# Optimization experiments

Measured on AMD Instinct MI355X. Metric: run time of the kernel, lower is better.

The kernel has to match this reference:

```python
import jax, jax.numpy as jnp
import numpy as np

Q_DIM = 64

def setup_inputs() -> dict:
    key = jax.random.key(0)
    k1, k2, k3, k4 = jax.random.split(key, 4)
    B, T, C, D = 2, 4096, 1024, Q_DIM
    x = jax.random.normal(k1, (B, T, C), dtype=jnp.float32)
    Wq = jax.random.normal(k2, (C, D), dtype=jnp.float32) * (C ** -0.5)
    Wk = jax.random.normal(k3, (C, D), dtype=jnp.float32) * (C ** -0.5)
    Wv = jax.random.normal(k4, (C, D), dtype=jnp.float32) * (C ** -0.5)
    return {"x": x, "Wq": Wq, "Wk": Wk, "Wv": Wv}

def reference(x, Wq, Wk, Wv):
    # x: [B,T,C]; Wq/Wk/Wv: [C,D]
    T = x.shape[1]
    D = Wq.shape[1]
    q = x @ Wq  # [B,T,D]
    k = x @ Wk
    v = x @ Wv
    scale = D ** -0.5
    aff = jnp.einsum('bqd,bkd->bqk', q, k) * scale  # [B,T,T]
    causal = jnp.tril(jnp.ones((T, T), dtype=bool))
    aff = jnp.where(causal, aff, -jnp.inf)
    attn = jax.nn.softmax(aff, axis=-1)
    out = jnp.einsum('bqk,bkd->bqd', attn, v)  # [B,T,D]
    return out
```

## Files before the change

kernel.cpp:

```cpp
#include <hip/hip_runtime.h>

typedef __bf16 bf16_t;
typedef __bf16 bf16x8 __attribute__((ext_vector_type(8)));
typedef __bf16 bf16x4 __attribute__((ext_vector_type(4)));
typedef float  f32x4  __attribute__((ext_vector_type(4)));
typedef _Float16 f16_t;
typedef _Float16 f16x8 __attribute__((ext_vector_type(8)));

#define TSEQ 4096
#define SEGS 8

__device__ __forceinline__ void barrier_lds() {
    __builtin_amdgcn_sched_barrier(0);
    asm volatile("s_waitcnt lgkmcnt(0)" ::: "memory");
    __builtin_amdgcn_s_barrier();
    __builtin_amdgcn_sched_barrier(0);
}

__global__ __launch_bounds__(256) void wsplit_k(
    const float* __restrict__ Wq, const float* __restrict__ Wk,
    const float* __restrict__ Wv, bf16_t* __restrict__ wT)
{
    __shared__ bf16_t th[64][72];
    const int mat = blockIdx.x >> 4;
    const int kb  = (blockIdx.x & 15) * 64;
    const float* W = (mat == 0) ? Wq : ((mat == 1) ? Wk : Wv);
    const float scale = (mat == 0) ? 0.18033688011112042f : 1.0f;
    const int t  = threadIdx.x;
    const int kl = t >> 2;
    const int dc = (t & 3) * 16;
    #pragma unroll
    for (int i = 0; i < 4; ++i) {
        float4 v = *reinterpret_cast<const float4*>(W + (long)(kb + kl) * 64 + dc + 4 * i);
        th[dc + 4*i + 0][kl] = (bf16_t)(v.x * scale);
        th[dc + 4*i + 1][kl] = (bf16_t)(v.y * scale);
        th[dc + 4*i + 2][kl] = (bf16_t)(v.z * scale);
        th[dc + 4*i + 3][kl] = (bf16_t)(v.w * scale);
    }
    __syncthreads();
    const int d  = t >> 2;
    const int kc = (t & 3) * 16;
    bf16x8 a0 = *reinterpret_cast<const bf16x8*>(&th[d][kc]);
    bf16x8 a1 = *reinterpret_cast<const bf16x8*>(&th[d][kc + 8]);
    long o = (long)(mat * 64 + d) * 1024 + kb + kc;
    *reinterpret_cast<bf16x8*>(wT + o)     = a0;
    *reinterpret_cast<bf16x8*>(wT + o + 8) = a1;
}

__global__ __launch_bounds__(256, 2) void proj_mfma(
    const float* __restrict__ X, const bf16_t* __restrict__ wT,
    bf16_t* __restrict__ qh, bf16_t* __restrict__ kh, bf16_t* __restrict__ vt)
{
    __shared__ __align__(16) unsigned char smem[13824];
    bf16_t (*wl)[48][72] = reinterpret_cast<bf16_t(*)[48][72]>(smem);
    float  (*vtl)[68]    = reinterpret_cast<float(*)[68]>(smem);

    const int tid = threadIdx.x, lane = tid & 63;
    const int mw  = tid >> 6;
    const int q4 = lane & 15, g = lane >> 4;
    const int bx = blockIdx.x;
    const int rg = bx & 127, nb = bx >> 7;
    const long R0 = (long)rg * 64;

    const float* xrow = X + (R0 + 16 * mw + q4) * 1024 + 8 * g;

    const int wrow = tid >> 2, c16 = (tid & 3) * 16;
    const bf16_t* wsrc = wT + (long)(48 * nb + wrow) * 1024 + c16;
    const bool wact = (tid < 192);

    bf16x8 wr0, wr1;
    float4 xE[4], xO[4];
    f32x4 acc[3] = {};

    auto loadW = [&](int t) {
        if (wact) {
            wr0 = *reinterpret_cast<const bf16x8*>(wsrc + t * 64);
            wr1 = *reinterpret_cast<const bf16x8*>(wsrc + t * 64 + 8);
        }
    };
    auto writeW = [&](int buf) {
        if (wact) {
            *reinterpret_cast<bf16x8*>(&wl[buf][wrow][c16])     = wr0;
            *reinterpret_cast<bf16x8*>(&wl[buf][wrow][c16 + 8]) = wr1;
        }
    };
    auto loadX = [&](int t, float4 (&xc)[4]) {
        xc[0] = *reinterpret_cast<const float4*>(xrow + t * 64);
        xc[1] = *reinterpret_cast<const float4*>(xrow + t * 64 + 4);
        xc[2] = *reinterpret_cast<const float4*>(xrow + t * 64 + 32);
        xc[3] = *reinterpret_cast<const float4*>(xrow + t * 64 + 36);
    };

    loadW(0); writeW(0);
    loadW(1);
    loadX(0, xE); loadX(1, xO);
    asm volatile("" ::: "memory");
    barrier_lds();

    auto stepf = [&](int t, float4 (&xc)[4]) {
        if (t + 1 < 16) {
            writeW((t + 1) & 1);
            loadW(t + 2 < 16 ? t + 2 : 15);
        }
        bf16x8 a0 = {(bf16_t)xc[0].x, (bf16_t)xc[0].y, (bf16_t)xc[0].z, (bf16_t)xc[0].w,
                     (bf16_t)xc[1].x, (bf16_t)xc[1].y, (bf16_t)xc[1].z, (bf16_t)xc[1].w};
        bf16x8 a1 = {(bf16_t)xc[2].x, (bf16_t)xc[2].y, (bf16_t)xc[2].z, (bf16_t)xc[2].w,
                     (bf16_t)xc[3].x, (bf16_t)xc[3].y, (bf16_t)xc[3].z, (bf16_t)xc[3].w};
        if (t + 2 < 16) loadX(t + 2, xc);
        asm volatile("" ::: "memory");
        __builtin_amdgcn_s_setprio(1);
        #pragma unroll
        for (int j = 0; j < 3; ++j) {
            bf16x8 b0 = *reinterpret_cast<const bf16x8*>(&wl[t & 1][16 * j + q4][8 * g]);
            bf16x8 b1 = *reinterpret_cast<const bf16x8*>(&wl[t & 1][16 * j + q4][8 * g + 32]);
            acc[j] = __builtin_amdgcn_mfma_f32_16x16x32_bf16(a0, b0, acc[j], 0, 0, 0);
            acc[j] = __builtin_amdgcn_mfma_f32_16x16x32_bf16(a1, b1, acc[j], 0, 0, 0);
        }
        __builtin_amdgcn_s_setprio(0);
        barrier_lds();
    };
    #pragma unroll
    for (int tt = 0; tt < 16; tt += 2) { stepf(tt, xE); stepf(tt + 1, xO); }

    const int vbase = (nb == 2) ? 0 : 16;
    #pragma unroll
    for (int j = 0; j < 3; ++j) {
        const int nt = 3 * nb + j;
        #pragma unroll
        for (int r = 0; r < 4; ++r) {
            const long row = R0 + 16 * mw + 4 * g + r;
            const float vv = acc[j][r];
            if (nt < 4)      qh[row * 64 + nt * 16 + q4] = (bf16_t)vv;
            else if (nt < 8) kh[row * 64 + (nt - 4) * 16 + q4] = (bf16_t)vv;
            else             vtl[(nt - 8) * 16 + q4 - vbase][16 * mw + 4 * g + r] = vv;
        }
    }
    if (nb >= 2) {
        barrier_lds();
        const int nd = (nb == 2) ? 16 : 48;
        const int dl = tid >> 2, cc = (tid & 3) * 16;
        if (dl < nd) {
            bf16x8 o0, o1;
            #pragma unroll
            for (int i = 0; i < 8; ++i) {
                o0[i] = (bf16_t)vtl[dl][cc + i];
                o1[i] = (bf16_t)vtl[dl][cc + 8 + i];
            }
            bf16_t* dst = vt + (long)(vbase + dl) * 8192 + R0 + cc;
            *reinterpret_cast<bf16x8*>(dst)     = o0;
            *reinterpret_cast<bf16x8*>(dst + 8) = o1;
        }
    }
}

__global__ __launch_bounds__(256, 3) void attn_mfma(
    const bf16_t* __restrict__ qh, const bf16_t* __restrict__ kh,
    const bf16_t* __restrict__ vt,
    f16_t* __restrict__ pO, float* __restrict__ pm, float* __restrict__ pl)
{
    __shared__ __align__(16) unsigned char smem[46080];
    bf16_t (*kl)[64][72]  = reinterpret_cast<bf16_t(*)[64][72]>(smem);
    bf16_t (*vl)[64][72]  = reinterpret_cast<bf16_t(*)[64][72]>(smem + 18432);
    bf16_t (*P)[8][16][8] = reinterpret_cast<bf16_t(*)[8][16][8]>(smem + 36864);
    f16_t  (*ot)[16][72]  = reinterpret_cast<f16_t(*)[16][72]>(smem + 36864);

    const int tid = threadIdx.x, lane = tid & 63, w = tid >> 6;
    const int q4 = lane & 15, g = lane >> 4;
    const int bx = blockIdx.x, b = blockIdx.y;
    const int tile = 63 - (bx >> 3);
    const int seg  = bx & 7;
    const int C = tile + 1;
    if (seg >= C) return;
    const long base = (long)b * TSEQ;
    const int r0 = tile * 64 + 16 * w;

    const bf16_t* qr = qh + (base + r0 + q4) * 64 + 8 * g;
    const bf16x8 qf0 = *reinterpret_cast<const bf16x8*>(qr);
    const bf16x8 qf1 = *reinterpret_cast<const bf16x8*>(qr + 32);

    const int srow = tid >> 2, sc = (tid & 3) * 16;
    const bf16_t* ksrc = kh + (base + srow) * 64 + sc;
    const bf16_t* vsrc = vt + (long)srow * 8192 + base + sc;
    bf16x8 kr0, kr1, vr0, vr1;
    auto loadKV = [&](int kb) {
        kr0 = *reinterpret_cast<const bf16x8*>(ksrc + (long)kb * 64);
        kr1 = *reinterpret_cast<const bf16x8*>(ksrc + (long)kb * 64 + 8);
        vr0 = *reinterpret_cast<const bf16x8*>(vsrc + kb);
        vr1 = *reinterpret_cast<const bf16x8*>(vsrc + kb + 8);
    };
    auto writeKV = [&](int buf) {
        *reinterpret_cast<bf16x8*>(&kl[buf][srow][sc])     = kr0;
        *reinterpret_cast<bf16x8*>(&kl[buf][srow][sc + 8]) = kr1;
        *reinterpret_cast<bf16x8*>(&vl[buf][srow][sc])     = vr0;
        *reinterpret_cast<bf16x8*>(&vl[buf][srow][sc + 8]) = vr1;
    };

    float m = -1e30f, l = 0.f;
    f32x4 oacc[4] = {};

    loadKV(seg << 6);
    writeKV(0);
    { int c1 = seg + SEGS; loadKV((c1 < C ? c1 : seg) << 6); }
    asm volatile("" ::: "memory");
    barrier_lds();

    int i = 0;
    for (int c = seg; c < C; c += SEGS, ++i) {
        const int buf = i & 1;
        if (c + SEGS < C) {
            writeKV(buf ^ 1);
            int cn = c + 2 * SEGS;
            loadKV((cn < C ? cn : c + SEGS) << 6);
            asm volatile("" ::: "memory");
        }
        const int kb = c << 6;

        f32x4 sacc[4];
        __builtin_amdgcn_s_setprio(1);
        #pragma unroll
        for (int kt = 0; kt < 4; ++kt) {
            bf16x8 kf0 = *reinterpret_cast<const bf16x8*>(&kl[buf][kt * 16 + q4][8 * g]);
            bf16x8 kf1 = *reinterpret_cast<const bf16x8*>(&kl[buf][kt * 16 + q4][8 * g + 32]);
            f32x4 a = {};
            a = __builtin_amdgcn_mfma_f32_16x16x32_bf16(kf0, qf0, a, 0, 0, 0);
            a = __builtin_amdgcn_mfma_f32_16x16x32_bf16(kf1, qf1, a, 0, 0, 0);
            sacc[kt] = a;
        }
        __builtin_amdgcn_s_setprio(0);

        float p[16];
        const bool diag = (c == C - 1);
        float mx = -1e30f;
        #pragma unroll
        for (int kt = 0; kt < 4; ++kt)
            #pragma unroll
            for (int r = 0; r < 4; ++r) {
                float sv = sacc[kt][r];
                if (diag && (kb + kt * 16 + 4 * g + r > r0 + q4)) sv = -1e30f;
                p[kt * 4 + r] = sv;
                mx = fmaxf(mx, sv);
            }
        mx = fmaxf(mx, __shfl_xor(mx, 16));
        mx = fmaxf(mx, __shfl_xor(mx, 32));
        const float mnew = fmaxf(m, mx);
        const float alpha = __builtin_exp2f(m - mnew);
        m = mnew;
        float lsum = 0.f;
        #pragma unroll
        for (int ii = 0; ii < 16; ++ii) { p[ii] = __builtin_exp2f(p[ii] - mnew); lsum += p[ii]; }
        lsum += __shfl_xor(lsum, 16);
        lsum += __shfl_xor(lsum, 32);
        l = l * alpha + lsum;
        #pragma unroll
        for (int dt = 0; dt < 4; ++dt) oacc[dt] *= alpha;

        #pragma unroll
        for (int kt = 0; kt < 4; ++kt) {
            const int cb = 2 * kt + (g >> 1);
            const int ki = (g & 1) << 2;
            bf16x4 hv = {(bf16_t)p[4*kt+0], (bf16_t)p[4*kt+1],
                         (bf16_t)p[4*kt+2], (bf16_t)p[4*kt+3]};
            *reinterpret_cast<bf16x4*>(&P[w][cb][q4][ki]) = hv;
        }
        bf16x8 ph0 = *reinterpret_cast<const bf16x8*>(&P[w][g][q4][0]);
        bf16x8 ph1 = *reinterpret_cast<const bf16x8*>(&P[w][4 + g][q4][0]);
        __builtin_amdgcn_s_setprio(1);
        #pragma unroll
        for (int dt = 0; dt < 4; ++dt) {
            bf16x8 va0 = *reinterpret_cast<const bf16x8*>(&vl[buf][dt * 16 + q4][8 * g]);
            bf16x8 va1 = *reinterpret_cast<const bf16x8*>(&vl[buf][dt * 16 + q4][8 * g + 32]);
            oacc[dt] = __builtin_amdgcn_mfma_f32_16x16x32_bf16(va0, ph0, oacc[dt], 0, 0, 0);
            oacc[dt] = __builtin_amdgcn_mfma_f32_16x16x32_bf16(va1, ph1, oacc[dt], 0, 0, 0);
        }
        __builtin_amdgcn_s_setprio(0);
        barrier_lds();
    }

    const float invl = 1.0f / l;
    #pragma unroll
    for (int dt = 0; dt < 4; ++dt)
        #pragma unroll
        for (int r = 0; r < 4; ++r)
            ot[w][q4][dt * 16 + 4 * g + r] = (f16_t)(oacc[dt][r] * invl);

    const long pbase = (((long)b * 64 + tile) * SEGS + seg) * 64;
    {
        const int q  = lane >> 2;
        const int dc = (lane & 3) * 16;
        f16x8 o0 = *reinterpret_cast<const f16x8*>(&ot[w][q][dc]);
        f16x8 o1 = *reinterpret_cast<const f16x8*>(&ot[w][q][dc + 8]);
        f16_t* dst = pO + (pbase + 16 * w + q) * 64 + dc;
        *reinterpret_cast<f16x8*>(dst)     = o0;
        *reinterpret_cast<f16x8*>(dst + 8) = o1;
    }
    if (g == 0) {
        pm[pbase + 16 * w + q4] = m;
        pl[pbase + 16 * w + q4] = l;
    }
}

__global__ __launch_bounds__(256) void merge_k(
    const f16_t* __restrict__ pO, const float* __restrict__ pm,
    const float* __restrict__ pl, float* __restrict__ O)
{
    const int tile = blockIdx.x, b = blockIdx.y;
    const int C = tile + 1;
    const int S = (C < SEGS) ? C : SEGS;
    const int t = threadIdx.x;
    const int q = t >> 2, dc = (t & 3) * 16;
    const long pb = ((long)b * 64 + tile) * SEGS;

    float mstar = -1e30f;
    for (int s = 0; s < S; ++s) mstar = fmaxf(mstar, pm[(pb + s) * 64 + q]);
    float L = 0.f;
    float o[16];
    #pragma unroll
    for (int i = 0; i < 16; ++i) o[i] = 0.f;
    for (int s = 0; s < S; ++s) {
        const float ws = __builtin_exp2f(pm[(pb + s) * 64 + q] - mstar) * pl[(pb + s) * 64 + q];
        L += ws;
        const f16_t* src = pO + ((pb + s) * 64 + q) * 64 + dc;
        f16x8 a0 = *reinterpret_cast<const f16x8*>(src);
        f16x8 a1 = *reinterpret_cast<const f16x8*>(src + 8);
        #pragma unroll
        for (int i = 0; i < 8; ++i) {
            o[i]     += ws * (float)a0[i];
            o[8 + i] += ws * (float)a1[i];
        }
    }
    const float inv = 1.0f / L;
    float* dst = O + ((long)b * TSEQ + tile * 64 + q) * 64 + dc;
    #pragma unroll
    for (int i = 0; i < 4; ++i) {
        f32x4 v = {o[4*i] * inv, o[4*i+1] * inv, o[4*i+2] * inv, o[4*i+3] * inv};
        *reinterpret_cast<f32x4*>(dst + 4 * i) = v;
    }
}

extern "C" void kernel_launch(void* const* d_in, const int* in_sizes, int n_in,
                              void* d_out, int out_size, void* d_ws, size_t ws_size,
                              hipStream_t stream)
{
    const float* X  = (const float*)d_in[0];
    const float* Wq = (const float*)d_in[1];
    const float* Wk = (const float*)d_in[2];
    const float* Wv = (const float*)d_in[3];
    float* O = (float*)d_out;

    char* ws = (char*)d_ws;
    size_t off = 0;
    bf16_t* wT = (bf16_t*)(ws + off); off += 192 * 1024 * sizeof(bf16_t);
    bf16_t* qh = (bf16_t*)(ws + off); off += 8192L * 64 * sizeof(bf16_t);
    bf16_t* kh = (bf16_t*)(ws + off); off += 8192L * 64 * sizeof(bf16_t);
    bf16_t* vt = (bf16_t*)(ws + off); off += 64L * 8192 * sizeof(bf16_t);
    f16_t*  pO = (f16_t*)(ws + off);  off += 2L * 64 * SEGS * 64 * 64 * sizeof(f16_t);
    float*  pm = (float*)(ws + off);  off += 2L * 64 * SEGS * 64 * sizeof(float);
    float*  pl = (float*)(ws + off);  off += 2L * 64 * SEGS * 64 * sizeof(float);

    wsplit_k <<<48, 256, 0, stream>>>(Wq, Wk, Wv, wT);
    proj_mfma<<<512, 256, 0, stream>>>(X, wT, qh, kh, vt);
    attn_mfma<<<dim3(512, 2), 256, 0, stream>>>(qh, kh, vt, pO, pm, pl);
    merge_k  <<<dim3(64, 2), 256, 0, stream>>>(pO, pm, pl, O);
}
```

Measured before the change: 52.85 us.

## Use single-wave attention blocks with K/V held in registers instead of LDS

```diff
diff --git a/kernel.cpp b/kernel.cpp
--- a/kernel.cpp
+++ b/kernel.cpp
@@ -6,6 +6,7 @@
 typedef float  f32x4  __attribute__((ext_vector_type(4)));
 typedef _Float16 f16_t;
 typedef _Float16 f16x8 __attribute__((ext_vector_type(8)));
+typedef _Float16 f16x4 __attribute__((ext_vector_type(4)));
 
 #define TSEQ 4096
 #define SEGS 8
@@ -153,127 +154,130 @@
     }
 }
 
-__global__ __launch_bounds__(256, 3) void attn_mfma(
+__global__ __launch_bounds__(64, 4) void attn_mfma(
     const bf16_t* __restrict__ qh, const bf16_t* __restrict__ kh,
     const bf16_t* __restrict__ vt,
     f16_t* __restrict__ pO, float* __restrict__ pm, float* __restrict__ pl)
 {
-    __shared__ __align__(16) unsigned char smem[46080];
-    bf16_t (*kl)[64][72]  = reinterpret_cast<bf16_t(*)[64][72]>(smem);
-    bf16_t (*vl)[64][72]  = reinterpret_cast<bf16_t(*)[64][72]>(smem + 18432);
-    bf16_t (*P)[8][16][8] = reinterpret_cast<bf16_t(*)[8][16][8]>(smem + 36864);
-    f16_t  (*ot)[16][72]  = reinterpret_cast<f16_t(*)[16][72]>(smem + 36864);
-
-    const int tid = threadIdx.x, lane = tid & 63, w = tid >> 6;
+    __shared__ __align__(16) unsigned char smem[2304];
+    bf16_t (*P)[16][8] = reinterpret_cast<bf16_t(*)[16][8]>(smem);
+    f16_t  (*ot)[72]   = reinterpret_cast<f16_t(*)[72]>(smem);
+
+    const int lane = threadIdx.x;
     const int q4 = lane & 15, g = lane >> 4;
-    const int bx = blockIdx.x, b = blockIdx.y;
-    const int tile = 63 - (bx >> 3);
-    const int seg  = bx & 7;
-    const int C = tile + 1;
+    const int bx = blockIdx.x;
+    const int b = bx >> 11;
+    const int inner = bx & 2047;
+    const int qi = 255 - (inner >> 3);
+    const int seg = inner & 7;
+    const int C = (qi >> 2) + 1;
     if (seg >= C) return;
     const long base = (long)b * TSEQ;
-    const int r0 = tile * 64 + 16 * w;
+    const int r0 = qi << 4;
 
     const bf16_t* qr = qh + (base + r0 + q4) * 64 + 8 * g;
     const bf16x8 qf0 = *reinterpret_cast<const bf16x8*>(qr);
     const bf16x8 qf1 = *reinterpret_cast<const bf16x8*>(qr + 32);
 
-    const int srow = tid >> 2, sc = (tid & 3) * 16;
-    const bf16_t* ksrc = kh + (base + srow) * 64 + sc;
-    const bf16_t* vsrc = vt + (long)srow * 8192 + base + sc;
-    bf16x8 kr0, kr1, vr0, vr1;
-    auto loadKV = [&](int kb) {
-        kr0 = *reinterpret_cast<const bf16x8*>(ksrc + (long)kb * 64);
-        kr1 = *reinterpret_cast<const bf16x8*>(ksrc + (long)kb * 64 + 8);
-        vr0 = *reinterpret_cast<const bf16x8*>(vsrc + kb);
-        vr1 = *reinterpret_cast<const bf16x8*>(vsrc + kb + 8);
-    };
-    auto writeKV = [&](int buf) {
-        *reinterpret_cast<bf16x8*>(&kl[buf][srow][sc])     = kr0;
-        *reinterpret_cast<bf16x8*>(&kl[buf][srow][sc + 8]) = kr1;
-        *reinterpret_cast<bf16x8*>(&vl[buf][srow][sc])     = vr0;
-        *reinterpret_cast<bf16x8*>(&vl[buf][srow][sc + 8]) = vr1;
+    bf16x8 kf[4][2], vf[4][2];
+    auto loadK = [&](int kb) {
+        #pragma unroll
+        for (int kt = 0; kt < 4; ++kt) {
+            const bf16_t* kr = kh + (base + kb + kt * 16 + q4) * 64 + 8 * g;
+            kf[kt][0] = *reinterpret_cast<const bf16x8*>(kr);
+            kf[kt][1] = *reinterpret_cast<const bf16x8*>(kr + 32);
+        }
+    };
+    auto loadV = [&](int kb) {
+        #pragma unroll
+        for (int dt = 0; dt < 4; ++dt) {
+            const bf16_t* vr = vt + (long)(dt * 16 + q4) * 8192 + base + kb + 8 * g;
+            vf[dt][0] = *reinterpret_cast<const bf16x8*>(vr);
+            vf[dt][1] = *reinterpret_cast<const bf16x8*>(vr + 32);
+        }
     };
 
     float m = -1e30f, l = 0.f;
     f32x4 oacc[4] = {};
 
-    loadKV(seg << 6);
-    writeKV(0);
-    { int c1 = seg + SEGS; loadKV((c1 < C ? c1 : seg) << 6); }
-    asm volatile("" ::: "memory");
-    barrier_lds();
-
-    int i = 0;
-    for (int c = seg; c < C; c += SEGS, ++i) {
-        const int buf = i & 1;
+    loadK(seg << 6);
+
+    for (int c = seg; c < C; c += SEGS) {
+        const int kb = c << 6;
+        loadV(kb);
+        asm volatile("" ::: "memory");
+
+        f32x4 sacc[4];
+        #pragma unroll
+        for (int kt = 0; kt < 4; ++kt) {
+            f32x4 a = {};
+            a = __builtin_amdgcn_mfma_f32_16x16x32_bf16(kf[kt][0], qf0, a, 0, 0, 0);
+            a = __builtin_amdgcn_mfma_f32_16x16x32_bf16(kf[kt][1], qf1, a, 0, 0, 0);
+            sacc[kt] = a;
+        }
         if (c + SEGS < C) {
-            writeKV(buf ^ 1);
-            int cn = c + 2 * SEGS;
-            loadKV((cn < C ? cn : c + SEGS) << 6);
+            loadK((c + SEGS) << 6);
             asm volatile("" ::: "memory");
         }
-        const int kb = c << 6;
-
-        f32x4 sacc[4];
-        __builtin_amdgcn_s_setprio(1);
-        #pragma unroll
-        for (int kt = 0; kt < 4; ++kt) {
-            bf16x8 kf0 = *reinterpret_cast<const bf16x8*>(&kl[buf][kt * 16 + q4][8 * g]);
-            bf16x8 kf1 = *reinterpret_cast<const bf16x8*>(&kl[buf][kt * 16 + q4][8 * g + 32]);
-            f32x4 a = {};
-            a = __builtin_amdgcn_mfma_f32_16x16x32_bf16(kf0, qf0, a, 0, 0, 0);
-            a = __builtin_amdgcn_mfma_f32_16x16x32_bf16(kf1, qf1, a, 0, 0, 0);
-            sacc[kt] = a;
-        }
-        __builtin_amdgcn_s_setprio(0);
-
-        float p[16];
-        const bool diag = (c == C - 1);
-        float mx = -1e30f;
+
+        if (c == C - 1) {
+            #pragma unroll
+            for (int kt = 0; kt < 4; ++kt)
+                #pragma unroll
+                for (int r = 0; r < 4; ++r)
+                    if (kb + kt * 16 + 4 * g + r > r0 + q4) sacc[kt][r] = -1e30f;
+        }
+
+        float mx = sacc[0][0];
         #pragma unroll
         for (int kt = 0; kt < 4; ++kt)
             #pragma unroll
-            for (int r = 0; r < 4; ++r) {
-                float sv = sacc[kt][r];
-                if (diag && (kb + kt * 16 + 4 * g + r > r0 + q4)) sv = -1e30f;
-                p[kt * 4 + r] = sv;
-                mx = fmaxf(mx, sv);
-            }
+            for (int r = 0; r < 4; ++r) mx = fmaxf(mx, sacc[kt][r]);
         mx = fmaxf(mx, __shfl_xor(mx, 16));
         mx = fmaxf(mx, __shfl_xor(mx, 32));
-        const float mnew = fmaxf(m, mx);
-        const float alpha = __builtin_exp2f(m - mnew);
-        m = mnew;
+
         float lsum = 0.f;
-        #pragma unroll
-        for (int ii = 0; ii < 16; ++ii) { p[ii] = __builtin_exp2f(p[ii] - mnew); lsum += p[ii]; }
+        if (__all(mx <= m)) {
+            #pragma unroll
+            for (int kt = 0; kt < 4; ++kt)
+                #pragma unroll
+                for (int r = 0; r < 4; ++r) {
+                    float e = __builtin_exp2f(sacc[kt][r] - m);
+                    sacc[kt][r] = e; lsum += e;
+                }
+        } else {
+            const float mnew = fmaxf(m, mx);
+            const float alpha = __builtin_exp2f(m - mnew);
+            m = mnew;
+            #pragma unroll
+            for (int kt = 0; kt < 4; ++kt)
+                #pragma unroll
+                for (int r = 0; r < 4; ++r) {
+                    float e = __builtin_exp2f(sacc[kt][r] - mnew);
+                    sacc[kt][r] = e; lsum += e;
+                }
+            #pragma unroll
+            for (int dt = 0; dt < 4; ++dt) oacc[dt] *= alpha;
+            l *= alpha;
+        }
         lsum += __shfl_xor(lsum, 16);
         lsum += __shfl_xor(lsum, 32);
-        l = l * alpha + lsum;
-        #pragma unroll
-        for (int dt = 0; dt < 4; ++dt) oacc[dt] *= alpha;
+        l += lsum;
 
         #pragma unroll
         for (int kt = 0; kt < 4; ++kt) {
-            const int cb = 2 * kt + (g >> 1);
-            const int ki = (g & 1) << 2;
-            bf16x4 hv = {(bf16_t)p[4*kt+0], (bf16_t)p[4*kt+1],
-                         (bf16_t)p[4*kt+2], (bf16_t)p[4*kt+3]};
-            *reinterpret_cast<bf16x4*>(&P[w][cb][q4][ki]) = hv;
-        }
-        bf16x8 ph0 = *reinterpret_cast<const bf16x8*>(&P[w][g][q4][0]);
-        bf16x8 ph1 = *reinterpret_cast<const bf16x8*>(&P[w][4 + g][q4][0]);
-        __builtin_amdgcn_s_setprio(1);
+            bf16x4 hv = {(bf16_t)sacc[kt][0], (bf16_t)sacc[kt][1],
+                         (bf16_t)sacc[kt][2], (bf16_t)sacc[kt][3]};
+            *reinterpret_cast<bf16x4*>(&P[2 * kt + (g >> 1)][q4][(g & 1) << 2]) = hv;
+        }
+        bf16x8 ph0 = *reinterpret_cast<const bf16x8*>(&P[g][q4][0]);
+        bf16x8 ph1 = *reinterpret_cast<const bf16x8*>(&P[4 + g][q4][0]);
+
         #pragma unroll
         for (int dt = 0; dt < 4; ++dt) {
-            bf16x8 va0 = *reinterpret_cast<const bf16x8*>(&vl[buf][dt * 16 + q4][8 * g]);
-            bf16x8 va1 = *reinterpret_cast<const bf16x8*>(&vl[buf][dt * 16 + q4][8 * g + 32]);
-            oacc[dt] = __builtin_amdgcn_mfma_f32_16x16x32_bf16(va0, ph0, oacc[dt], 0, 0, 0);
-            oacc[dt] = __builtin_amdgcn_mfma_f32_16x16x32_bf16(va1, ph1, oacc[dt], 0, 0, 0);
-        }
-        __builtin_amdgcn_s_setprio(0);
-        barrier_lds();
+            oacc[dt] = __builtin_amdgcn_mfma_f32_16x16x32_bf16(vf[dt][0], ph0, oacc[dt], 0, 0, 0);
+            oacc[dt] = __builtin_amdgcn_mfma_f32_16x16x32_bf16(vf[dt][1], ph1, oacc[dt], 0, 0, 0);
+        }
     }
 
     const float invl = 1.0f / l;
@@ -281,21 +285,21 @@
     for (int dt = 0; dt < 4; ++dt)
         #pragma unroll
         for (int r = 0; r < 4; ++r)
-            ot[w][q4][dt * 16 + 4 * g + r] = (f16_t)(oacc[dt][r] * invl);
-
-    const long pbase = (((long)b * 64 + tile) * SEGS + seg) * 64;
+            ot[q4][dt * 16 + 4 * g + r] = (f16_t)(oacc[dt][r] * invl);
+
+    const long pb = ((long)b * 256 + qi) * SEGS + seg;
     {
         const int q  = lane >> 2;
-        const int dc = (lane & 3) * 16;
-        f16x8 o0 = *reinterpret_cast<const f16x8*>(&ot[w][q][dc]);
-        f16x8 o1 = *reinterpret_cast<const f16x8*>(&ot[w][q][dc + 8]);
-        f16_t* dst = pO + (pbase + 16 * w + q) * 64 + dc;
+        const int dc = (lane & 3) << 4;
+        f16x8 o0 = *reinterpret_cast<const f16x8*>(&ot[q][dc]);
+        f16x8 o1 = *reinterpret_cast<const f16x8*>(&ot[q][dc + 8]);
+        f16_t* dst = pO + (pb * 16 + q) * 64 + dc;
         *reinterpret_cast<f16x8*>(dst)     = o0;
         *reinterpret_cast<f16x8*>(dst + 8) = o1;
     }
     if (g == 0) {
-        pm[pbase + 16 * w + q4] = m;
-        pl[pbase + 16 * w + q4] = l;
+        pm[pb * 16 + q4] = m;
+        pl[pb * 16 + q4] = l;
     }
 }
 
@@ -304,37 +308,27 @@
     const float* __restrict__ pl, float* __restrict__ O)
 {
     const int tile = blockIdx.x, b = blockIdx.y;
-    const int C = tile + 1;
+    const int C = (tile >> 2) + 1;
     const int S = (C < SEGS) ? C : SEGS;
     const int t = threadIdx.x;
-    const int q = t >> 2, dc = (t & 3) * 16;
-    const long pb = ((long)b * 64 + tile) * SEGS;
+    const int q = t >> 4, dc = (t & 15) << 2;
+    const long pb = ((long)b * 256 + tile) * SEGS;
 
     float mstar = -1e30f;
-    for (int s = 0; s < S; ++s) mstar = fmaxf(mstar, pm[(pb + s) * 64 + q]);
+    for (int s = 0; s < S; ++s) mstar = fmaxf(mstar, pm[(pb + s) * 16 + q]);
     float L = 0.f;
-    float o[16];
-    #pragma unroll
-    for (int i = 0; i < 16; ++i) o[i] = 0.f;
+    float o[4] = {0.f, 0.f, 0.f, 0.f};
     for (int s = 0; s < S; ++s) {
-        const float ws = __builtin_exp2f(pm[(pb + s) * 64 + q] - mstar) * pl[(pb + s) * 64 + q];
+        const float ws = __builtin_exp2f(pm[(pb + s) * 16 + q] - mstar) * pl[(pb + s) * 16 + q];
         L += ws;
-        const f16_t* src = pO + ((pb + s) * 64 + q) * 64 + dc;
-        f16x8 a0 = *reinterpret_cast<const f16x8*>(src);
-        f16x8 a1 = *reinterpret_cast<const f16x8*>(src + 8);
-        #pragma unroll
-        for (int i = 0; i < 8; ++i) {
-            o[i]     += ws * (float)a0[i];
-            o[8 + i] += ws * (float)a1[i];
-        }
+        const f16_t* src = pO + ((pb + s) * 16 + q) * 64 + dc;
+        f16x4 a = *reinterpret_cast<const f16x4*>(src);
+        #pragma unroll
+        for (int i = 0; i < 4; ++i) o[i] += ws * (float)a[i];
     }
     const float inv = 1.0f / L;
-    float* dst = O + ((long)b * TSEQ + tile * 64 + q) * 64 + dc;
-    #pragma unroll
-    for (int i = 0; i < 4; ++i) {
-        f32x4 v = {o[4*i] * inv, o[4*i+1] * inv, o[4*i+2] * inv, o[4*i+3] * inv};
-        *reinterpret_cast<f32x4*>(dst + 4 * i) = v;
-    }
+    f32x4 v = {o[0] * inv, o[1] * inv, o[2] * inv, o[3] * inv};
+    *reinterpret_cast<f32x4*>(O + ((long)b * TSEQ + tile * 16 + q) * 64 + dc) = v;
 }
 
 extern "C" void kernel_launch(void* const* d_in, const int* in_sizes, int n_in,
@@ -353,12 +347,12 @@
     bf16_t* qh = (bf16_t*)(ws + off); off += 8192L * 64 * sizeof(bf16_t);
     bf16_t* kh = (bf16_t*)(ws + off); off += 8192L * 64 * sizeof(bf16_t);
     bf16_t* vt = (bf16_t*)(ws + off); off += 64L * 8192 * sizeof(bf16_t);
-    f16_t*  pO = (f16_t*)(ws + off);  off += 2L * 64 * SEGS * 64 * 64 * sizeof(f16_t);
-    float*  pm = (float*)(ws + off);  off += 2L * 64 * SEGS * 64 * sizeof(float);
-    float*  pl = (float*)(ws + off);  off += 2L * 64 * SEGS * 64 * sizeof(float);
+    f16_t*  pO = (f16_t*)(ws + off);  off += 2L * 256 * SEGS * 16 * 64 * sizeof(f16_t);
+    float*  pm = (float*)(ws + off);  off += 2L * 256 * SEGS * 16 * sizeof(float);
+    float*  pl = (float*)(ws + off);  off += 2L * 256 * SEGS * 16 * sizeof(float);
 
     wsplit_k <<<48, 256, 0, stream>>>(Wq, Wk, Wv, wT);
     proj_mfma<<<512, 256, 0, stream>>>(X, wT, qh, kh, vt);
-    attn_mfma<<<dim3(512, 2), 256, 0, stream>>>(qh, kh, vt, pO, pm, pl);
-    merge_k  <<<dim3(64, 2), 256, 0, stream>>>(pO, pm, pl, O);
-}
+    attn_mfma<<<dim3(4096), 64, 0, stream>>>(qh, kh, vt, pO, pm, pl);
+    merge_k  <<<dim3(256, 2), 256, 0, stream>>>(pO, pm, pl, O);
+}
```

Measured after the change: 97.19 us. 1.84x slower.

## Retile QKV projection to 32-row blocks covering 96 output columns

Applied to the files above, without the earlier changes.

```diff
diff --git a/kernel.cpp b/kernel.cpp
--- a/kernel.cpp
+++ b/kernel.cpp
@@ -51,24 +51,25 @@
     const float* __restrict__ X, const bf16_t* __restrict__ wT,
     bf16_t* __restrict__ qh, bf16_t* __restrict__ kh, bf16_t* __restrict__ vt)
 {
-    __shared__ __align__(16) unsigned char smem[13824];
-    bf16_t (*wl)[48][72] = reinterpret_cast<bf16_t(*)[48][72]>(smem);
-    float  (*vtl)[68]    = reinterpret_cast<float(*)[68]>(smem);
+    __shared__ __align__(16) unsigned char smem[27648];
+    bf16_t (*wl)[96][72] = reinterpret_cast<bf16_t(*)[96][72]>(smem);
+    float  (*vtl)[36]    = reinterpret_cast<float(*)[36]>(smem);
 
     const int tid = threadIdx.x, lane = tid & 63;
-    const int mw  = tid >> 6;
+    const int w   = tid >> 6;
+    const int mw  = w >> 1, nw2 = w & 1;
     const int q4 = lane & 15, g = lane >> 4;
     const int bx = blockIdx.x;
-    const int rg = bx & 127, nb = bx >> 7;
-    const long R0 = (long)rg * 64;
+    const int rg = bx & 255, nb = bx >> 8;
+    const long R0 = (long)rg * 32;
 
     const float* xrow = X + (R0 + 16 * mw + q4) * 1024 + 8 * g;
 
-    const int wrow = tid >> 2, c16 = (tid & 3) * 16;
-    const bf16_t* wsrc = wT + (long)(48 * nb + wrow) * 1024 + c16;
+    const int wrow = tid >> 1, c32 = (tid & 1) * 32;
+    const bf16_t* wsrc = wT + (long)(96 * nb + wrow) * 1024 + c32;
     const bool wact = (tid < 192);
 
-    bf16x8 wr0, wr1;
+    bf16x8 wr0, wr1, wr2, wr3;
     float4 xE[4], xO[4];
     f32x4 acc[3] = {};
 
@@ -76,12 +77,16 @@
         if (wact) {
             wr0 = *reinterpret_cast<const bf16x8*>(wsrc + t * 64);
             wr1 = *reinterpret_cast<const bf16x8*>(wsrc + t * 64 + 8);
+            wr2 = *reinterpret_cast<const bf16x8*>(wsrc + t * 64 + 16);
+            wr3 = *reinterpret_cast<const bf16x8*>(wsrc + t * 64 + 24);
         }
     };
     auto writeW = [&](int buf) {
         if (wact) {
-            *reinterpret_cast<bf16x8*>(&wl[buf][wrow][c16])     = wr0;
-            *reinterpret_cast<bf16x8*>(&wl[buf][wrow][c16 + 8]) = wr1;
+            *reinterpret_cast<bf16x8*>(&wl[buf][wrow][c32])      = wr0;
+            *reinterpret_cast<bf16x8*>(&wl[buf][wrow][c32 + 8])  = wr1;
+            *reinterpret_cast<bf16x8*>(&wl[buf][wrow][c32 + 16]) = wr2;
+            *reinterpret_cast<bf16x8*>(&wl[buf][wrow][c32 + 24]) = wr3;
         }
     };
     auto loadX = [&](int t, float4 (&xc)[4]) {
@@ -111,8 +116,9 @@
         __builtin_amdgcn_s_setprio(1);
         #pragma unroll
         for (int j = 0; j < 3; ++j) {
-            bf16x8 b0 = *reinterpret_cast<const bf16x8*>(&wl[t & 1][16 * j + q4][8 * g]);
-            bf16x8 b1 = *reinterpret_cast<const bf16x8*>(&wl[t & 1][16 * j + q4][8 * g + 32]);
+            const int lr = (3 * nw2 + j) * 16 + q4;
+            bf16x8 b0 = *reinterpret_cast<const bf16x8*>(&wl[t & 1][lr][8 * g]);
+            bf16x8 b1 = *reinterpret_cast<const bf16x8*>(&wl[t & 1][lr][8 * g + 32]);
             acc[j] = __builtin_amdgcn_mfma_f32_16x16x32_bf16(a0, b0, acc[j], 0, 0, 0);
             acc[j] = __builtin_amdgcn_mfma_f32_16x16x32_bf16(a1, b1, acc[j], 0, 0, 0);
         }
@@ -122,34 +128,25 @@
     #pragma unroll
     for (int tt = 0; tt < 16; tt += 2) { stepf(tt, xE); stepf(tt + 1, xO); }
 
-    const int vbase = (nb == 2) ? 0 : 16;
     #pragma unroll
     for (int j = 0; j < 3; ++j) {
-        const int nt = 3 * nb + j;
+        const int nt = 6 * nb + 3 * nw2 + j;
         #pragma unroll
         for (int r = 0; r < 4; ++r) {
             const long row = R0 + 16 * mw + 4 * g + r;
             const float vv = acc[j][r];
             if (nt < 4)      qh[row * 64 + nt * 16 + q4] = (bf16_t)vv;
             else if (nt < 8) kh[row * 64 + (nt - 4) * 16 + q4] = (bf16_t)vv;
-            else             vtl[(nt - 8) * 16 + q4 - vbase][16 * mw + 4 * g + r] = vv;
-        }
-    }
-    if (nb >= 2) {
+            else             vtl[(nt - 8) * 16 + q4][16 * mw + 4 * g + r] = vv;
+        }
+    }
+    if (nb == 1) {
         barrier_lds();
-        const int nd = (nb == 2) ? 16 : 48;
-        const int dl = tid >> 2, cc = (tid & 3) * 16;
-        if (dl < nd) {
-            bf16x8 o0, o1;
-            #pragma unroll
-            for (int i = 0; i < 8; ++i) {
-                o0[i] = (bf16_t)vtl[dl][cc + i];
-                o1[i] = (bf16_t)vtl[dl][cc + 8 + i];
-            }
-            bf16_t* dst = vt + (long)(vbase + dl) * 8192 + R0 + cc;
-            *reinterpret_cast<bf16x8*>(dst)     = o0;
-            *reinterpret_cast<bf16x8*>(dst + 8) = o1;
-        }
+        const int d = tid >> 2, c8 = (tid & 3) * 8;
+        bf16x8 o;
+        #pragma unroll
+        for (int i = 0; i < 8; ++i) o[i] = (bf16_t)vtl[d][c8 + i];
+        *reinterpret_cast<bf16x8*>(vt + (long)d * 8192 + R0 + c8) = o;
     }
 }
 
```

New measurement: 57.80 us. 1.09x slower.
